# Performance work log

Hardware: AMD Instinct MI355X
Metric: run time of the kernel (lower is better)

## Reference

```python
import jax, jax.numpy as jnp
import numpy as np

N_NODES = 50000
N_EDGES = 600000
D_IN = 128
D_HID = 128


def _graph_conv(x, src, dst, W, b, n_nodes):
    # DGL GraphConv with norm='both': out = D_in^{-1/2} A (D_out^{-1/2} x) W + b
    ones = jnp.ones(src.shape[0], dtype=x.dtype)
    deg_out = jnp.maximum(jax.ops.segment_sum(ones, src, num_segments=n_nodes), 1.0)
    deg_in = jnp.maximum(jax.ops.segment_sum(ones, dst, num_segments=n_nodes), 1.0)
    h = x * (deg_out ** -0.5)[:, None]            # [N, d] scale by src-side norm
    agg = jax.ops.segment_sum(h[src], dst, num_segments=n_nodes)  # SpMM aggregate
    agg = agg * (deg_in ** -0.5)[:, None]
    return agg @ W + b


def _two_layer(x, src, dst, W1, b1, W2, b2):
    h = jax.nn.relu(_graph_conv(x, src, dst, W1, b1, N_NODES))
    return jax.nn.relu(_graph_conv(h, src, dst, W2, b2, N_NODES))


def setup_inputs() -> dict:
    key = jax.random.key(0)
    ks = jax.random.split(key, 16)
    inp = {}
    for i in range(4):
        inp[f"x{i+1}"] = jax.random.normal(ks[3 * i], (N_NODES, D_IN), dtype=jnp.float32)
        inp[f"src{i+1}"] = jax.random.randint(ks[3 * i + 1], (N_EDGES,), 0, N_NODES)
        inp[f"dst{i+1}"] = jax.random.randint(ks[3 * i + 2], (N_EDGES,), 0, N_NODES)
    inp["W1"] = jax.random.normal(ks[12], (D_IN, D_HID), dtype=jnp.float32) * (D_IN ** -0.5)
    inp["b1"] = jnp.zeros((D_HID,), dtype=jnp.float32)
    inp["W2"] = jax.random.normal(ks[13], (D_HID, D_HID), dtype=jnp.float32) * (D_HID ** -0.5)
    inp["b2"] = jnp.zeros((D_HID,), dtype=jnp.float32)
    return inp


def reference(x1, src1, dst1, x2, src2, dst2, x3, src3, dst3, x4, src4, dst4,
              W1, b1, W2, b2):
    h1 = _two_layer(x1, src1, dst1, W1, b1, W2, b2)
    h2 = _two_layer(x2, src2, dst2, W1, b1, W2, b2)
    h3 = _two_layer(x3, src3, dst3, W1, b1, W2, b2)
    h4 = _two_layer(x4, src4, dst4, W1, b1, W2, b2)
    # multi_graph_opt='mean': concat along node axis, mean over nodes -> [D_HID]
    x = jnp.mean(jnp.concatenate([h1, h2, h3, h4], axis=0), axis=0)
    # output_opt='mean': scalar
    return jnp.mean(x)
```

## Files before the change

### kernel.cpp

```cpp
#include <hip/hip_runtime.h>
#include <hip/hip_bf16.h>

#define N_NODES 50000
#define N_EDGES 600000
#define D 128

#define NBUCK 64
#define BUCK_R 782
#define BCAP 16384
#define EPB 2048

typedef __attribute__((ext_vector_type(8))) short bf16x8;
typedef __attribute__((ext_vector_type(4))) float f32x4;
typedef __attribute__((ext_vector_type(2))) float f32x2;

__device__ __forceinline__ const int* pick4(const int* a, const int* b,
                                            const int* c, const int* d, int g) {
    return g == 0 ? a : g == 1 ? b : g == 2 ? c : d;
}
__device__ __forceinline__ const float4* pick4f(const float4* a, const float4* b,
                                                const float4* c, const float4* d, int g) {
    return g == 0 ? a : g == 1 ? b : g == 2 ? c : d;
}

__device__ __forceinline__ unsigned bfpair(float a, float b) {
    unsigned ua = __float_as_uint(a); ua = (ua + 0x7FFF + ((ua >> 16) & 1)) >> 16;
    unsigned ub = __float_as_uint(b); ub = (ub + 0x7FFF + ((ub >> 16) & 1)) >> 16;
    return ua | (ub << 16);
}

__global__ __launch_bounds__(256) void phaseA_kernel(
        const int* s0, const int* s1, const int* s2, const int* s3,
        const int* d0, const int* d1, const int* d2, const int* d3,
        int* __restrict__ bCurD, int* __restrict__ bCurS,
        int* __restrict__ pairs, unsigned short* __restrict__ svals, int nEdges) {
    int gi = blockIdx.y;
    const int* src = pick4(s0, s1, s2, s3, gi);
    const int* dst = pick4(d0, d1, d2, d3, gi);
    int* pg = pairs + (size_t)gi * NBUCK * BCAP;
    unsigned short* sg = svals + (size_t)gi * NBUCK * BCAP;

    __shared__ int cntD[64], cntS[64], gposD[64], gposS[64], lcurD[64], lcurS[64];
    int t = threadIdx.x;
    if (t < 64) { cntD[t] = 0; cntS[t] = 0; }
    __syncthreads();

    int myD[8], myS[8];
    int base = blockIdx.x * EPB + t;
    #pragma unroll
    for (int j = 0; j < 8; ++j) {
        int e = base + j * 256;
        if (e < nEdges) {
            myD[j] = dst[e]; myS[j] = src[e];
            atomicAdd(&cntD[myD[j] / BUCK_R], 1);
            atomicAdd(&cntS[myS[j] / BUCK_R], 1);
        } else myD[j] = -1;
    }
    __syncthreads();
    if (t < 64) {
        int c = cntD[t];
        gposD[t] = t * BCAP + (c ? atomicAdd(&bCurD[gi * 64 + t], c) : 0);
        lcurD[t] = 0;
        c = cntS[t];
        gposS[t] = t * BCAP + (c ? atomicAdd(&bCurS[gi * 64 + t], c) : 0);
        lcurS[t] = 0;
    }
    __syncthreads();
    #pragma unroll
    for (int j = 0; j < 8; ++j) {
        if (myD[j] >= 0) {
            int bD = myD[j] / BUCK_R, bS = myS[j] / BUCK_R;
            int lp = atomicAdd(&lcurD[bD], 1);
            pg[gposD[bD] + lp] = ((myD[j] - bD * BUCK_R) << 16) | myS[j];
            int ls = atomicAdd(&lcurS[bS], 1);
            sg[gposS[bS] + ls] = (unsigned short)(myS[j] - bS * BUCK_R);
        }
    }
}

__global__ __launch_bounds__(256) void csrB_kernel(
        const int* __restrict__ bCurD, const int* __restrict__ pairs,
        int* __restrict__ rowptrBase, int* __restrict__ eixBase,
        float* __restrict__ rsIBase) {
    int gi = blockIdx.y, b = blockIdx.x;
    int* rowptr = rowptrBase + (size_t)gi * (N_NODES + 1);
    int* eidx = eixBase + (size_t)gi * N_EDGES;
    float* rsI = rsIBase + (size_t)gi * N_NODES;
    const int* pg = pairs + ((size_t)gi * NBUCK + b) * BCAP;
    const int* bCur = bCurD + gi * 64;

    __shared__ int P[BCAP];
    __shared__ int cnt[1024];
    __shared__ int cur[1024];
    __shared__ int wpart[4];
    __shared__ int sbase;

    int t = threadIdx.x;
    int nb = bCur[b]; if (nb > BCAP) nb = BCAP;

    if (t < 64) {
        int v = (t < b) ? min(bCur[t], BCAP) : 0;
        for (int off = 32; off; off >>= 1) v += __shfl_down(v, off, 64);
        if (t == 0) sbase = v;
    }
    for (int i = t; i < 1024; i += 256) cnt[i] = 0;
    __syncthreads();
    int base = sbase;

    for (int i = t; i < nb; i += 256) {
        int p = pg[i];
        P[i] = p;
        atomicAdd(&cnt[p >> 16], 1);
    }
    __syncthreads();

    int c0 = cnt[t * 4 + 0], c1 = cnt[t * 4 + 1], c2 = cnt[t * 4 + 2], c3 = cnt[t * 4 + 3];
    int ts = c0 + c1 + c2 + c3;
    int lane = t & 63, w = t >> 6;
    int incl = ts;
    for (int off = 1; off < 64; off <<= 1) {
        int u = __shfl_up(incl, off, 64);
        if (lane >= off) incl += u;
    }
    if (lane == 63) wpart[w] = incl;
    __syncthreads();
    int wb = 0;
    #pragma unroll
    for (int i = 0; i < 4; ++i) if (i < w) wb += wpart[i];
    int ex = wb + incl - ts;
    cur[t * 4 + 0] = ex;
    cur[t * 4 + 1] = ex + c0;
    cur[t * 4 + 2] = ex + c0 + c1;
    cur[t * 4 + 3] = ex + c0 + c1 + c2;
    __syncthreads();

    int lo = b * BUCK_R;
    int nh = N_NODES - lo; if (nh > BUCK_R) nh = BUCK_R;
    for (int i = t; i < nh; i += 256) {
        rowptr[lo + i] = base + cur[i];
        rsI[lo + i] = 1.0f / sqrtf(fmaxf((float)cnt[i], 1.0f));
    }
    if (b == NBUCK - 1 && t == 0) rowptr[N_NODES] = N_EDGES;
    __syncthreads();

    for (int i = t; i < nb; i += 256) {
        int p = P[i];
        int pos = atomicAdd(&cur[p >> 16], 1);
        eidx[base + pos] = p & 0xFFFF;
    }
}

__global__ __launch_bounds__(256) void csrC_kernel(
        const int* __restrict__ bCurS, const unsigned short* __restrict__ svals,
        float* __restrict__ rsOBase) {
    int gi = blockIdx.y, b = blockIdx.x;
    float* rsO = rsOBase + (size_t)gi * N_NODES;
    const unsigned short* sg = svals + ((size_t)gi * NBUCK + b) * BCAP;
    __shared__ int cnt[1024];
    int t = threadIdx.x;
    for (int i = t; i < 1024; i += 256) cnt[i] = 0;
    __syncthreads();
    int ns = bCurS[gi * 64 + b]; if (ns > BCAP) ns = BCAP;
    for (int i = t; i < ns; i += 256) atomicAdd(&cnt[sg[i]], 1);
    __syncthreads();
    int lo = b * BUCK_R;
    int nh = N_NODES - lo; if (nh > BUCK_R) nh = BUCK_R;
    for (int i = t; i < nh; i += 256)
        rsO[lo + i] = 1.0f / sqrtf(fmaxf((float)cnt[i], 1.0f));
}

__global__ void wconv_kernel(const float* __restrict__ W1, const float* __restrict__ W2,
                             unsigned* __restrict__ Wp1, unsigned* __restrict__ Wp2) {
    const float* W = blockIdx.y ? W2 : W1;
    unsigned* Wp = blockIdx.y ? Wp2 : Wp1;
    int o = blockIdx.x * 256 + threadIdx.x;
    int j2 = o & 3, lane = (o >> 2) & 63, nt = (o >> 8) & 7, kc = o >> 11;
    int k = kc * 32 + (lane >> 4) * 8 + j2 * 2;
    int col = nt * 16 + (lane & 15);
    Wp[o] = bfpair(W[k * 128 + col], W[(k + 1) * 128 + col]);
}

__global__ void xconv_kernel(const float4* x0, const float4* x1,
                             const float4* x2, const float4* x3,
                             const float* __restrict__ rsOBase,
                             uint2* __restrict__ xbBase, int gFirst, int n ) {
    int gi = blockIdx.y;
    const float4* x = pick4f(x0, x1, x2, x3, gFirst + gi);
    const float* rsO = rsOBase + (size_t)(gFirst + gi) * N_NODES;
    uint2* xb = xbBase + (size_t)gi * (N_NODES * 16);
    int i = blockIdx.x * blockDim.x + threadIdx.x;
    if (i >= n) return;
    float sc = rsO[i >> 4];
    float4 a = x[i * 2];
    float4 b = x[i * 2 + 1];
    int w0 = __builtin_amdgcn_cvt_pk_fp8_f32(a.x * sc, a.y * sc, 0, false);
    w0 = __builtin_amdgcn_cvt_pk_fp8_f32(a.z * sc, a.w * sc, w0, true);
    int w1 = __builtin_amdgcn_cvt_pk_fp8_f32(b.x * sc, b.y * sc, 0, false);
    w1 = __builtin_amdgcn_cvt_pk_fp8_f32(b.z * sc, b.w * sc, w1, true);
    xb[i] = make_uint2((unsigned)w0, (unsigned)w1);
}

#define NCHUNK 3125
template <int LAYER>
__global__ __launch_bounds__(256) void fused_kernel(
        const int* __restrict__ rowptrBase, const int* __restrict__ eixBase,
        const unsigned char* __restrict__ hBase,
        const float* __restrict__ rsIBase, const float* __restrict__ rsOBase,
        const uint4* __restrict__ Wp, const float* __restrict__ bias,
        unsigned char* __restrict__ outBase, double* __restrict__ acc, int gFirst) {
    const int gi = blockIdx.y;
    const int g = gFirst + gi;
    const int* rowptr = rowptrBase + (size_t)g * (N_NODES + 1);
    const int* eidx   = eixBase + (size_t)g * N_EDGES;
    const float* rsI  = rsIBase + (size_t)g * N_NODES;
    const float* rsO  = rsOBase + (size_t)g * N_NODES;
    const unsigned char* h = hBase + (size_t)gi * N_NODES * D;
    unsigned char* outb = outBase + (size_t)gi * N_NODES * D;

    __shared__ unsigned short A[16][136];

    const int t = threadIdx.x;
    const int row = t >> 4;
    const int sub = t & 15;
    const int lane = t & 63, wv = t >> 6;
    const int l15 = lane & 15, lh = lane >> 4;

    bf16x8 bfr[4][2];
    #pragma unroll
    for (int kc = 0; kc < 4; ++kc)
        #pragma unroll
        for (int j = 0; j < 2; ++j) {
            uint4 u = Wp[(kc * 8 + wv * 2 + j) * 64 + lane];
            bfr[kc][j] = *(bf16x8*)&u;
        }
    float bv[2];
    #pragma unroll
    for (int j = 0; j < 2; ++j) bv[j] = bias[wv * 32 + j * 16 + l15];

    double lsum = 0.0;

    for (int ch = blockIdx.x; ch < NCHUNK; ch += gridDim.x) {
        const int r = ch * 16 + row;
        float a[8] = {0.f, 0.f, 0.f, 0.f, 0.f, 0.f, 0.f, 0.f};
        int p = rowptr[r], pend = rowptr[r + 1];
        const unsigned char* hp = h + sub * 8;
        for (; p + 2 <= pend; p += 2) {
            uint2 u = *(const uint2*)(hp + (size_t)eidx[p] * 128);
            uint2 v = *(const uint2*)(hp + (size_t)eidx[p + 1] * 128);
            f32x2 c0 = __builtin_amdgcn_cvt_pk_f32_fp8(u.x, false);
            f32x2 c1 = __builtin_amdgcn_cvt_pk_f32_fp8(u.x, true);
            f32x2 c2 = __builtin_amdgcn_cvt_pk_f32_fp8(u.y, false);
            f32x2 c3 = __builtin_amdgcn_cvt_pk_f32_fp8(u.y, true);
            a[0] += c0[0]; a[1] += c0[1]; a[2] += c1[0]; a[3] += c1[1];
            a[4] += c2[0]; a[5] += c2[1]; a[6] += c3[0]; a[7] += c3[1];
            f32x2 d0 = __builtin_amdgcn_cvt_pk_f32_fp8(v.x, false);
            f32x2 d1 = __builtin_amdgcn_cvt_pk_f32_fp8(v.x, true);
            f32x2 d2 = __builtin_amdgcn_cvt_pk_f32_fp8(v.y, false);
            f32x2 d3 = __builtin_amdgcn_cvt_pk_f32_fp8(v.y, true);
            a[0] += d0[0]; a[1] += d0[1]; a[2] += d1[0]; a[3] += d1[1];
            a[4] += d2[0]; a[5] += d2[1]; a[6] += d3[0]; a[7] += d3[1];
        }
        if (p < pend) {
            uint2 u = *(const uint2*)(hp + (size_t)eidx[p] * 128);
            f32x2 c0 = __builtin_amdgcn_cvt_pk_f32_fp8(u.x, false);
            f32x2 c1 = __builtin_amdgcn_cvt_pk_f32_fp8(u.x, true);
            f32x2 c2 = __builtin_amdgcn_cvt_pk_f32_fp8(u.y, false);
            f32x2 c3 = __builtin_amdgcn_cvt_pk_f32_fp8(u.y, true);
            a[0] += c0[0]; a[1] += c0[1]; a[2] += c1[0]; a[3] += c1[1];
            a[4] += c2[0]; a[5] += c2[1]; a[6] += c3[0]; a[7] += c3[1];
        }
        {
            float sc = rsI[r];
            uint4 pk;
            pk.x = bfpair(a[0] * sc, a[1] * sc);
            pk.y = bfpair(a[2] * sc, a[3] * sc);
            pk.z = bfpair(a[4] * sc, a[5] * sc);
            pk.w = bfpair(a[6] * sc, a[7] * sc);
            *(uint4*)&A[row][sub * 8] = pk;
        }
        __syncthreads();

        bf16x8 afr[4];
        #pragma unroll
        for (int kc = 0; kc < 4; ++kc) {
            uint4 u = *(const uint4*)&A[l15][kc * 32 + lh * 8];
            afr[kc] = *(bf16x8*)&u;
        }
        __syncthreads();

        f32x4 c[2];
        c[0] = (f32x4){0.f, 0.f, 0.f, 0.f};
        c[1] = (f32x4){0.f, 0.f, 0.f, 0.f};
        #pragma unroll
        for (int kc = 0; kc < 4; ++kc) {
            c[0] = __builtin_amdgcn_mfma_f32_16x16x32_bf16(afr[kc], bfr[kc][0], c[0], 0, 0, 0);
            c[1] = __builtin_amdgcn_mfma_f32_16x16x32_bf16(afr[kc], bfr[kc][1], c[1], 0, 0, 0);
        }

        const int r0 = ch * 16 + lh * 4;
        if (LAYER == 2) {
            #pragma unroll
            for (int jj = 0; jj < 4; ++jj) {
                lsum += (double)fmaxf(c[0][jj] + bv[0], 0.f)
                      + (double)fmaxf(c[1][jj] + bv[1], 0.f);
            }
        } else {
            #pragma unroll
            for (int jj = 0; jj < 4; ++jj) {
                int rr = r0 + jj;
                if (rr < N_NODES) {
                    float sc = rsO[rr];
                    float o0 = fmaxf(c[0][jj] + bv[0], 0.f) * sc;
                    float o1 = fmaxf(c[1][jj] + bv[1], 0.f) * sc;
                    unsigned b0 = (unsigned)__builtin_amdgcn_cvt_pk_fp8_f32(o0, o0, 0, false);
                    unsigned b1 = (unsigned)__builtin_amdgcn_cvt_pk_fp8_f32(o1, o1, 0, false);
                    outb[(size_t)rr * 128 + wv * 32 + l15]      = (unsigned char)(b0 & 0xFF);
                    outb[(size_t)rr * 128 + wv * 32 + 16 + l15] = (unsigned char)(b1 & 0xFF);
                }
            }
        }
    }

    if (LAYER == 2) {
        for (int off = 32; off; off >>= 1) lsum += __shfl_down(lsum, off, 64);
        __shared__ double wred[4];
        if (lane == 0) wred[wv] = lsum;
        __syncthreads();
        if (t == 0) atomicAdd(acc, wred[0] + wred[1] + wred[2] + wred[3]);
    }
}

__global__ void finalize_kernel(const double* __restrict__ acc, float* __restrict__ out) {
    if (threadIdx.x == 0 && blockIdx.x == 0)
        out[0] = (float)(acc[0] / (4.0 * N_NODES * D));
}

extern "C" void kernel_launch(void* const* d_in, const int* in_sizes, int n_in,
                              void* d_out, int out_size, void* d_ws, size_t ws_size,
                              hipStream_t stream) {
    const float* x[4];
    const int* src[4];
    const int* dst[4];
    for (int g = 0; g < 4; ++g) {
        x[g]   = (const float*)d_in[3 * g + 0];
        src[g] = (const int*)  d_in[3 * g + 1];
        dst[g] = (const int*)  d_in[3 * g + 2];
    }
    const float* W1 = (const float*)d_in[12];
    const float* b1 = (const float*)d_in[13];
    const float* W2 = (const float*)d_in[14];
    const float* b2 = (const float*)d_in[15];
    float* out = (float*)d_out;

    int* ws32 = (int*)d_ws;
    double* acc     = (double*)d_ws;
    int* bCurD      = ws32 + 64;
    int* bCurS      = ws32 + 320;
    unsigned* Wp1   = (unsigned*)(ws32 + 1024);
    unsigned* Wp2   = Wp1 + 8192;
    int* rowptrBase = ws32 + 17408;
    float* rsIBase  = (float*)(ws32 + 217412);
    float* rsOBase  = (float*)(ws32 + 417412);
    int* eixBase    = ws32 + 617412;
    int* pairs      = ws32 + 3017412;
    unsigned short* svals = (unsigned short*)(pairs + 4194304);
    unsigned char* xbA    = (unsigned char*)(ws32 + 3017412);

    auto needBytes = [](int gb) -> size_t {
        size_t ov = (size_t)gb * 3200000;
        if (ov < 6291456) ov = 6291456;
        return (3017412 + ov) * 4;
    };
    int gb = 1;
    if (ws_size >= needBytes(4)) gb = 4;
    else if (ws_size >= needBytes(2)) gb = 2;
    unsigned char* AbA = xbA + (size_t)gb * N_NODES * D;

    const int paGrid    = (N_EDGES + EPB - 1) / EPB;
    const int xconvGrid = (N_NODES * 16 + 255) / 256;
    const int fusedGrid = 1563;

    hipMemsetAsync(d_ws, 0, 1024 * sizeof(int), stream);

    wconv_kernel<<<dim3(32, 2), 256, 0, stream>>>(W1, W2, Wp1, Wp2);
    phaseA_kernel<<<dim3(paGrid, 4), 256, 0, stream>>>(
        src[0], src[1], src[2], src[3], dst[0], dst[1], dst[2], dst[3],
        bCurD, bCurS, pairs, svals, N_EDGES);
    csrB_kernel<<<dim3(NBUCK, 4), 256, 0, stream>>>(
        bCurD, pairs, rowptrBase, eixBase, rsIBase);
    csrC_kernel<<<dim3(NBUCK, 4), 256, 0, stream>>>(bCurS, svals, rsOBase);

    for (int g0 = 0; g0 < 4; g0 += gb) {
        int nb = 4 - g0 < gb ? 4 - g0 : gb;
        xconv_kernel<<<dim3(xconvGrid, nb), 256, 0, stream>>>(
            (const float4*)x[0], (const float4*)x[1], (const float4*)x[2], (const float4*)x[3],
            rsOBase, (uint2*)xbA, g0, N_NODES * 16);
        fused_kernel<1><<<dim3(fusedGrid, nb), 256, 0, stream>>>(
            rowptrBase, eixBase, xbA, rsIBase, rsOBase,
            (const uint4*)Wp1, b1, AbA, nullptr, g0);
        fused_kernel<2><<<dim3(fusedGrid, nb), 256, 0, stream>>>(
            rowptrBase, eixBase, AbA, rsIBase, rsOBase,
            (const uint4*)Wp2, b2, nullptr, acc, g0);
    }

    finalize_kernel<<<1, 64, 0, stream>>>(acc, out);
}
```

Before: 307.9 us.

## Process 32 rows per block with 16-byte fp8 gathers and unroll-by-4

Each fused block now handles one 32-row chunk instead of looping over 16-row chunks. Each thread gathers 16 fp8 bytes per neighbor rather than 8, so 8 threads cover a row and 32 rows are in flight per block. The edge loop is unrolled by 4 to put more gathers in flight, and the block runs two 16-row MFMA tiles. In exchange it uses more registers for 16 accumulators and drops the grid-stride loop, so weight-fragment loads are no longer amortised over several chunks.

```diff
diff --git a/kernel.cpp b/kernel.cpp
--- a/kernel.cpp
+++ b/kernel.cpp
@@ -200,7 +200,24 @@
     xb[i] = make_uint2((unsigned)w0, (unsigned)w1);
 }
 
-#define NCHUNK 3125
+#define NCH32 1563
+
+#define ACC16(U)                                                            \
+    {                                                                       \
+        f32x2 e0 = __builtin_amdgcn_cvt_pk_f32_fp8((U).x, false);           \
+        f32x2 e1 = __builtin_amdgcn_cvt_pk_f32_fp8((U).x, true);            \
+        f32x2 e2 = __builtin_amdgcn_cvt_pk_f32_fp8((U).y, false);           \
+        f32x2 e3 = __builtin_amdgcn_cvt_pk_f32_fp8((U).y, true);            \
+        f32x2 e4 = __builtin_amdgcn_cvt_pk_f32_fp8((U).z, false);           \
+        f32x2 e5 = __builtin_amdgcn_cvt_pk_f32_fp8((U).z, true);            \
+        f32x2 e6 = __builtin_amdgcn_cvt_pk_f32_fp8((U).w, false);           \
+        f32x2 e7 = __builtin_amdgcn_cvt_pk_f32_fp8((U).w, true);            \
+        a[0] += e0[0];  a[1] += e0[1];  a[2] += e1[0];  a[3] += e1[1];      \
+        a[4] += e2[0];  a[5] += e2[1];  a[6] += e3[0];  a[7] += e3[1];      \
+        a[8] += e4[0];  a[9] += e4[1];  a[10] += e5[0]; a[11] += e5[1];     \
+        a[12] += e6[0]; a[13] += e6[1]; a[14] += e7[0]; a[15] += e7[1];     \
+    }
+
 template <int LAYER>
 __global__ __launch_bounds__(256) void fused_kernel(
         const int* __restrict__ rowptrBase, const int* __restrict__ eixBase,
@@ -217,11 +234,11 @@
     const unsigned char* h = hBase + (size_t)gi * N_NODES * D;
     unsigned char* outb = outBase + (size_t)gi * N_NODES * D;
 
-    __shared__ unsigned short A[16][136];
+    __shared__ unsigned short A[32][136];
 
     const int t = threadIdx.x;
-    const int row = t >> 4;
-    const int sub = t & 15;
+    const int row = t >> 3;
+    const int sub = t & 7;
     const int lane = t & 63, wv = t >> 6;
     const int l15 = lane & 15, lh = lane >> 4;
 
@@ -237,83 +254,76 @@
     #pragma unroll
     for (int j = 0; j < 2; ++j) bv[j] = bias[wv * 32 + j * 16 + l15];
 
-    double lsum = 0.0;
-
-    for (int ch = blockIdx.x; ch < NCHUNK; ch += gridDim.x) {
-        const int r = ch * 16 + row;
-        float a[8] = {0.f, 0.f, 0.f, 0.f, 0.f, 0.f, 0.f, 0.f};
-        int p = rowptr[r], pend = rowptr[r + 1];
-        const unsigned char* hp = h + sub * 8;
-        for (; p + 2 <= pend; p += 2) {
-            uint2 u = *(const uint2*)(hp + (size_t)eidx[p] * 128);
-            uint2 v = *(const uint2*)(hp + (size_t)eidx[p + 1] * 128);
-            f32x2 c0 = __builtin_amdgcn_cvt_pk_f32_fp8(u.x, false);
-            f32x2 c1 = __builtin_amdgcn_cvt_pk_f32_fp8(u.x, true);
-            f32x2 c2 = __builtin_amdgcn_cvt_pk_f32_fp8(u.y, false);
-            f32x2 c3 = __builtin_amdgcn_cvt_pk_f32_fp8(u.y, true);
-            a[0] += c0[0]; a[1] += c0[1]; a[2] += c1[0]; a[3] += c1[1];
-            a[4] += c2[0]; a[5] += c2[1]; a[6] += c3[0]; a[7] += c3[1];
-            f32x2 d0 = __builtin_amdgcn_cvt_pk_f32_fp8(v.x, false);
-            f32x2 d1 = __builtin_amdgcn_cvt_pk_f32_fp8(v.x, true);
-            f32x2 d2 = __builtin_amdgcn_cvt_pk_f32_fp8(v.y, false);
-            f32x2 d3 = __builtin_amdgcn_cvt_pk_f32_fp8(v.y, true);
-            a[0] += d0[0]; a[1] += d0[1]; a[2] += d1[0]; a[3] += d1[1];
-            a[4] += d2[0]; a[5] += d2[1]; a[6] += d3[0]; a[7] += d3[1];
-        }
-        if (p < pend) {
-            uint2 u = *(const uint2*)(hp + (size_t)eidx[p] * 128);
-            f32x2 c0 = __builtin_amdgcn_cvt_pk_f32_fp8(u.x, false);
-            f32x2 c1 = __builtin_amdgcn_cvt_pk_f32_fp8(u.x, true);
-            f32x2 c2 = __builtin_amdgcn_cvt_pk_f32_fp8(u.y, false);
-            f32x2 c3 = __builtin_amdgcn_cvt_pk_f32_fp8(u.y, true);
-            a[0] += c0[0]; a[1] += c0[1]; a[2] += c1[0]; a[3] += c1[1];
-            a[4] += c2[0]; a[5] += c2[1]; a[6] += c3[0]; a[7] += c3[1];
-        }
-        {
-            float sc = rsI[r];
-            uint4 pk;
-            pk.x = bfpair(a[0] * sc, a[1] * sc);
-            pk.y = bfpair(a[2] * sc, a[3] * sc);
-            pk.z = bfpair(a[4] * sc, a[5] * sc);
-            pk.w = bfpair(a[6] * sc, a[7] * sc);
-            *(uint4*)&A[row][sub * 8] = pk;
-        }
-        __syncthreads();
-
-        bf16x8 afr[4];
+    const int ch = blockIdx.x;
+    const int r = ch * 32 + row;
+    int p = 0, pend = 0;
+    float sc = 0.f;
+    if (r < N_NODES) { p = rowptr[r]; pend = rowptr[r + 1]; sc = rsI[r]; }
+
+    float a[16];
+    #pragma unroll
+    for (int j = 0; j < 16; ++j) a[j] = 0.f;
+    const unsigned char* hp = h + sub * 16;
+    for (; p + 4 <= pend; p += 4) {
+        uint4 u0 = *(const uint4*)(hp + (size_t)eidx[p] * 128);
+        uint4 u1 = *(const uint4*)(hp + (size_t)eidx[p + 1] * 128);
+        uint4 u2 = *(const uint4*)(hp + (size_t)eidx[p + 2] * 128);
+        uint4 u3 = *(const uint4*)(hp + (size_t)eidx[p + 3] * 128);
+        ACC16(u0) ACC16(u1) ACC16(u2) ACC16(u3)
+    }
+    for (; p < pend; ++p) {
+        uint4 u0 = *(const uint4*)(hp + (size_t)eidx[p] * 128);
+        ACC16(u0)
+    }
+    {
+        uint4 pkA, pkB;
+        pkA.x = bfpair(a[0] * sc, a[1] * sc);
+        pkA.y = bfpair(a[2] * sc, a[3] * sc);
+        pkA.z = bfpair(a[4] * sc, a[5] * sc);
+        pkA.w = bfpair(a[6] * sc, a[7] * sc);
+        pkB.x = bfpair(a[8] * sc, a[9] * sc);
+        pkB.y = bfpair(a[10] * sc, a[11] * sc);
+        pkB.z = bfpair(a[12] * sc, a[13] * sc);
+        pkB.w = bfpair(a[14] * sc, a[15] * sc);
+        *(uint4*)&A[row][sub * 16]     = pkA;
+        *(uint4*)&A[row][sub * 16 + 8] = pkB;
+    }
+    __syncthreads();
+
+    f32x4 c[2][2];
+    #pragma unroll
+    for (int ti = 0; ti < 2; ++ti) {
+        c[ti][0] = (f32x4){0.f, 0.f, 0.f, 0.f};
+        c[ti][1] = (f32x4){0.f, 0.f, 0.f, 0.f};
+    }
+    #pragma unroll
+    for (int ti = 0; ti < 2; ++ti) {
         #pragma unroll
         for (int kc = 0; kc < 4; ++kc) {
-            uint4 u = *(const uint4*)&A[l15][kc * 32 + lh * 8];
-            afr[kc] = *(bf16x8*)&u;
+            uint4 u = *(const uint4*)&A[ti * 16 + l15][kc * 32 + lh * 8];
+            bf16x8 afr = *(bf16x8*)&u;
+            c[ti][0] = __builtin_amdgcn_mfma_f32_16x16x32_bf16(afr, bfr[kc][0], c[ti][0], 0, 0, 0);
+            c[ti][1] = __builtin_amdgcn_mfma_f32_16x16x32_bf16(afr, bfr[kc][1], c[ti][1], 0, 0, 0);
         }
-        __syncthreads();
-
-        f32x4 c[2];
-        c[0] = (f32x4){0.f, 0.f, 0.f, 0.f};
-        c[1] = (f32x4){0.f, 0.f, 0.f, 0.f};
+    }
+
+    double lsum = 0.0;
+    #pragma unroll
+    for (int ti = 0; ti < 2; ++ti) {
+        const int r0 = ch * 32 + ti * 16 + lh * 4;
         #pragma unroll
-        for (int kc = 0; kc < 4; ++kc) {
-            c[0] = __builtin_amdgcn_mfma_f32_16x16x32_bf16(afr[kc], bfr[kc][0], c[0], 0, 0, 0);
-            c[1] = __builtin_amdgcn_mfma_f32_16x16x32_bf16(afr[kc], bfr[kc][1], c[1], 0, 0, 0);
-        }
-
-        const int r0 = ch * 16 + lh * 4;
-        if (LAYER == 2) {
-            #pragma unroll
-            for (int jj = 0; jj < 4; ++jj) {
-                lsum += (double)fmaxf(c[0][jj] + bv[0], 0.f)
-                      + (double)fmaxf(c[1][jj] + bv[1], 0.f);
-            }
-        } else {
-            #pragma unroll
-            for (int jj = 0; jj < 4; ++jj) {
-                int rr = r0 + jj;
-                if (rr < N_NODES) {
-                    float sc = rsO[rr];
-                    float o0 = fmaxf(c[0][jj] + bv[0], 0.f) * sc;
-                    float o1 = fmaxf(c[1][jj] + bv[1], 0.f) * sc;
-                    unsigned b0 = (unsigned)__builtin_amdgcn_cvt_pk_fp8_f32(o0, o0, 0, false);
-                    unsigned b1 = (unsigned)__builtin_amdgcn_cvt_pk_fp8_f32(o1, o1, 0, false);
+        for (int jj = 0; jj < 4; ++jj) {
+            int rr = r0 + jj;
+            if (rr < N_NODES) {
+                float o0 = fmaxf(c[ti][0][jj] + bv[0], 0.f);
+                float o1 = fmaxf(c[ti][1][jj] + bv[1], 0.f);
+                if (LAYER == 2) {
+                    lsum += (double)o0 + (double)o1;
+                } else {
+                    float s2 = rsO[rr];
+                    float q0 = o0 * s2, q1 = o1 * s2;
+                    unsigned b0 = (unsigned)__builtin_amdgcn_cvt_pk_fp8_f32(q0, q0, 0, false);
+                    unsigned b1 = (unsigned)__builtin_amdgcn_cvt_pk_fp8_f32(q1, q1, 0, false);
                     outb[(size_t)rr * 128 + wv * 32 + l15]      = (unsigned char)(b0 & 0xFF);
                     outb[(size_t)rr * 128 + wv * 32 + 16 + l15] = (unsigned char)(b1 & 0xFF);
                 }
@@ -378,7 +388,6 @@
 
     const int paGrid    = (N_EDGES + EPB - 1) / EPB;
     const int xconvGrid = (N_NODES * 16 + 255) / 256;
-    const int fusedGrid = 1563;
 
     hipMemsetAsync(d_ws, 0, 1024 * sizeof(int), stream);
 
@@ -395,10 +404,10 @@
         xconv_kernel<<<dim3(xconvGrid, nb), 256, 0, stream>>>(
             (const float4*)x[0], (const float4*)x[1], (const float4*)x[2], (const float4*)x[3],
             rsOBase, (uint2*)xbA, g0, N_NODES * 16);
-        fused_kernel<1><<<dim3(fusedGrid, nb), 256, 0, stream>>>(
+        fused_kernel<1><<<dim3(NCH32, nb), 256, 0, stream>>>(
             rowptrBase, eixBase, xbA, rsIBase, rsOBase,
             (const uint4*)Wp1, b1, AbA, nullptr, g0);
-        fused_kernel<2><<<dim3(fusedGrid, nb), 256, 0, stream>>>(
+        fused_kernel<2><<<dim3(NCH32, nb), 256, 0, stream>>>(
             rowptrBase, eixBase, AbA, rsIBase, rsOBase,
             (const uint4*)Wp2, b2, nullptr, acc, g0);
     }
```

Measured after the change: 280.7 us. 1.1x faster.
